# Kernel optimization log

Hardware: AMD Instinct MI355X
Metric: run time of the kernel (lower is better)

## Reference

```python
import jax, jax.numpy as jnp
import numpy as np

B, NI, NP, A, R, D, SH = 1024, 256, 131072, 32, 8, 28, 9
WHITE_BKGD = True

C0 = 0.28209479177387814
C1 = 0.4886025119029199
C2 = (1.0925484305920792, -1.0925484305920792, 0.31539156525252005,
      -1.0925484305920792, 0.5462742152960396)

def sh_basis(dirs):
    # real SH basis, degree 2 (9 components), on normalized directions
    d = dirs / jnp.linalg.norm(dirs, axis=-1, keepdims=True)
    x, y, z = d[..., 0], d[..., 1], d[..., 2]
    return jnp.stack([
        jnp.full_like(x, C0), -C1 * y, C1 * z, -C1 * x,
        C2[0] * x * y, C2[1] * y * z, C2[2] * (2.0 * z * z - x * x - y * y),
        C2[3] * x * z, C2[4] * (x * x - y * y)], axis=-1)

def setup_inputs():
    key = jax.random.key(0)
    k0, k1, k2, k3, k4 = jax.random.split(key, 5)
    rays_d = jax.random.normal(k0, (B, 3), dtype=jnp.float32)
    queries = 0.1 * jax.random.normal(k1, (NP, A), dtype=jnp.float32)
    intrs_pts = jax.random.uniform(k2, (NP, 3), dtype=jnp.float32)
    intersections = 2.0 + 4.0 * jnp.sort(
        jax.random.uniform(k3, (B, NI + 1), dtype=jnp.float32), axis=1)
    atoms = 0.05 * jax.random.normal(k4, (A, R ** 3, D), dtype=jnp.float32)
    atoms = atoms.at[..., -1].add(0.1)  # init_sigma on density channel
    idx = np.sort(np.random.default_rng(0).choice(B * NI, NP, replace=False)).astype(np.int32)
    return {"rays_d": rays_d, "queries": queries, "intrs_pts": intrs_pts,
            "intersections": intersections, "atoms": atoms,
            "scatter_idx": jnp.asarray(idx)}

def reference(rays_d, queries, intrs_pts, intersections, atoms, scatter_idx):
    # ---- l2_interp: dictionary-atom trilinear interpolation ----
    pts = intrs_pts * 2.0 - 1.0                                  # [-1,1]^3 (in-place mul/sub in torch)
    coord = jnp.clip((pts + 1.0) * 0.5 * (R - 1), 0.0, R - 1)    # align_corners grid coords
    i0 = jnp.clip(jnp.floor(coord).astype(jnp.int32), 0, R - 2)
    f = coord - i0.astype(coord.dtype)                            # [NP,3] fractional offsets
    data = jnp.zeros((NP, D), dtype=queries.dtype)
    for dx in (0, 1):
        for dy in (0, 1):
            for dz in (0, 1):
                idx = ((i0[:, 0] + dx) * R + (i0[:, 1] + dy)) * R + (i0[:, 2] + dz)
                w = ((f[:, 0] if dx else 1.0 - f[:, 0]) *
                     (f[:, 1] if dy else 1.0 - f[:, 1]) *
                     (f[:, 2] if dz else 1.0 - f[:, 2]))
                g = atoms[:, idx, :]                              # [A, NP, D]
                data = data + jnp.einsum('pa,apd->pd', queries * w[:, None], g)
    # ---- density: masked_scatter + relu ----
    sigma_m = data[:, -1]
    sigma = jnp.zeros((B * NI,), sigma_m.dtype).at[scatter_idx].set(sigma_m).reshape(B, NI)
    sigma = jax.nn.relu(sigma)
    # ---- sigma2alpha: alpha compositing weights ----
    dists = jnp.diff(intersections, axis=1) * jnp.linalg.norm(rays_d, axis=-1, keepdims=True)
    alpha = 1.0 - jnp.exp(-sigma * dists)                         # [B, NI]
    trans = jnp.cumprod(1.0 - alpha + 1e-10, axis=1)
    trans = jnp.concatenate([jnp.ones((B, 1), alpha.dtype), trans[:, :-1]], axis=1)
    abs_light = alpha * trans
    # ---- SH shading on masked points ----
    sh_m = sh_basis(rays_d)[scatter_idx // NI]                    # [NP, SH] (gather via ray index)
    rgb_m = jnp.sum(sh_m[:, None, :] * data[:, :-1].reshape(NP, 3, SH), axis=-1)
    rgb = jnp.zeros((B * NI, 3), rgb_m.dtype).at[scatter_idx].set(rgb_m).reshape(B, NI, 3)
    # ---- shrgb2rgb ----
    rgb = jax.nn.sigmoid(rgb)
    acc = jnp.sum(abs_light, axis=1)
    rgb_out = jnp.sum(abs_light[..., None] * rgb, axis=1)
    if WHITE_BKGD:
        rgb_out = rgb_out + (1.0 - acc)[:, None]
    # ---- depth_map ----
    mid = 0.5 * (intersections[:, :-1] + intersections[:, 1:])
    depth = jnp.sum(abs_light * mid, axis=1)
    return rgb_out, alpha, depth
```

## Files before the change

kernel.cpp:

```cpp
#include <hip/hip_runtime.h>

#define NPTS  131072
#define NB    1024
#define NI    256
#define NA    32
#define RR    8
#define ND    28
#define NCELL 343
#define CAP   768
#define NCHUNKS 3
#define CHUNK 256

typedef _Float16 half8v __attribute__((ext_vector_type(8)));
typedef float    f32x4  __attribute__((ext_vector_type(4)));

__device__ __forceinline__ void cell_coords(const float* __restrict__ ip, int p,
                                            int& ix, int& iy, int& iz) {
  float cx = fminf(fmaxf(ip[p * 3 + 0] * 7.f, 0.f), 7.f);
  float cy = fminf(fmaxf(ip[p * 3 + 1] * 7.f, 0.f), 7.f);
  float cz = fminf(fmaxf(ip[p * 3 + 2] * 7.f, 0.f), 7.f);
  ix = (int)floorf(cx); ix = ix > 6 ? 6 : ix;
  iy = (int)floorf(cy); iy = iy > 6 ? 6 : iy;
  iz = (int)floorf(cz); iz = iz > 6 ? 6 : iz;
}

__global__ __launch_bounds__(256) void init_transpose(const float* __restrict__ atoms,
                                                      _Float16* __restrict__ atomsH,
                                                      f32x4* __restrict__ zbuf,
                                                      int* __restrict__ cnt) {
  int idx = blockIdx.x * 256 + threadIdx.x;
  int vox = idx >> 10;
  int d = (idx >> 5) & 31;
  int a = idx & 31;
  float v = 0.f;
  if (d < ND) v = atoms[(a * 512 + vox) * ND + d];
  atomsH[idx] = (_Float16)v;
  if (idx < NB * NI) {
    f32x4 z = {0.f, 0.f, 0.f, 0.f};
    zbuf[idx] = z;
  }
  if (idx < NCELL) cnt[idx] = 0;
}

__global__ __launch_bounds__(256) void scatter_kernel(const float* __restrict__ ip,
                                                      int* __restrict__ cnt,
                                                      int* __restrict__ perm) {
  __shared__ int sc[NCELL];
  __shared__ int sbase[NCELL];
  for (int c = threadIdx.x; c < NCELL; c += 256) sc[c] = 0;
  __syncthreads();
  int mycell[4], myrank[4], myp[4];
#pragma unroll
  for (int u = 0; u < 4; u++) {
    int p = blockIdx.x * 1024 + u * 256 + threadIdx.x;
    int ix, iy, iz;
    cell_coords(ip, p, ix, iy, iz);
    int cell = (ix * 7 + iy) * 7 + iz;
    mycell[u] = cell;
    myp[u] = p;
    myrank[u] = atomicAdd(&sc[cell], 1);
  }
  __syncthreads();
  for (int c = threadIdx.x; c < NCELL; c += 256) {
    int n = sc[c];
    sbase[c] = n ? atomicAdd(&cnt[c], n) : 0;
  }
  __syncthreads();
#pragma unroll
  for (int u = 0; u < 4; u++)
    perm[mycell[u] * CAP + sbase[mycell[u]] + myrank[u]] = myp[u];
}

__global__ __launch_bounds__(256) void gemm_points(
    const int* __restrict__ cnt, const int* __restrict__ perm,
    const float* __restrict__ queries, const float* __restrict__ intrs_pts,
    const float* __restrict__ rays_d, const int* __restrict__ scatter_idx,
    const _Float16* __restrict__ atomsH,
    float* __restrict__ sigma_d, float* __restrict__ rgb_d) {
  int cell = blockIdx.x / NCHUNKS;
  int chunk = blockIdx.x - cell * NCHUNKS;
  int n = cnt[cell];
  int s0 = chunk * CHUNK;
  if (s0 >= n) return;
  int e0 = min(n, s0 + CHUNK);
  const int* pcell = perm + cell * CAP;

  int cx = cell / 49, cy = (cell / 7) % 7, cz = cell % 7;

  __shared__ _Float16 Bs[8 * 32 * 32];
  __shared__ float Ds[4][16][33];

  int t = threadIdx.x;
#pragma unroll
  for (int u = 0; u < 4; u++) {
    int chk = t + u * 256;
    int g = chk << 3;
    int c = g >> 10;
    int rem = g & 1023;
    int d = rem >> 5;
    int kg = (rem >> 3) & 3;
    int vox = ((cx + (c >> 2)) * RR + cy + ((c >> 1) & 1)) * RR + cz + (c & 1);
    const _Float16* src = atomsH + vox * 1024 + d * 32 + (kg << 3);
    int swz = kg ^ ((d >> 1) & 3);
    _Float16* dst = (_Float16*)Bs + c * 1024 + d * 32 + (swz << 3);
    *(half8v*)dst = *(const half8v*)src;
  }
  __syncthreads();

  int lane = t & 63, w = t >> 6;
  int n0 = lane & 15, kg = lane >> 4;

  half8v Bf[8][2];
#pragma unroll
  for (int s = 0; s < 8; s++)
#pragma unroll
    for (int dt = 0; dt < 2; dt++) {
      int nn = n0 + 16 * dt;
      int swz = kg ^ ((nn >> 1) & 3);
      Bf[s][dt] = *(const half8v*)((const _Float16*)Bs + (s * 32 + nn) * 32 + (swz << 3));
    }

  for (int tile = 0; tile < 4; tile++) {
    int pbase = s0 + w * 64 + tile * 16;
    if (pbase >= e0) break;
    int pidx = pbase + n0;
    bool valid = pidx < e0;
    int p = valid ? pcell[pidx] : 0;

    float cxv = fminf(fmaxf(intrs_pts[p * 3 + 0] * 7.f, 0.f), 7.f);
    float cyv = fminf(fmaxf(intrs_pts[p * 3 + 1] * 7.f, 0.f), 7.f);
    float czv = fminf(fmaxf(intrs_pts[p * 3 + 2] * 7.f, 0.f), 7.f);
    float fx = cxv - (float)cx;
    float fy = cyv - (float)cy;
    float fz = czv - (float)cz;
    float vm = valid ? 1.f : 0.f;

    float wgt[8];
#pragma unroll
    for (int s = 0; s < 8; s++)
      wgt[s] = vm * ((s & 4) ? fx : 1.f - fx) * ((s & 2) ? fy : 1.f - fy) *
               ((s & 1) ? fz : 1.f - fz);

    f32x4 q0 = *(const f32x4*)(queries + p * NA + kg * 8);
    f32x4 q1 = *(const f32x4*)(queries + p * NA + kg * 8 + 4);
    half8v qh;
    qh[0] = (_Float16)q0[0]; qh[1] = (_Float16)q0[1];
    qh[2] = (_Float16)q0[2]; qh[3] = (_Float16)q0[3];
    qh[4] = (_Float16)q1[0]; qh[5] = (_Float16)q1[1];
    qh[6] = (_Float16)q1[2]; qh[7] = (_Float16)q1[3];

    f32x4 acc0 = {0.f, 0.f, 0.f, 0.f};
    f32x4 acc1 = {0.f, 0.f, 0.f, 0.f};
#pragma unroll
    for (int s = 0; s < 8; s++) {
      _Float16 wh = (_Float16)wgt[s];
      half8v ws8 = {wh, wh, wh, wh, wh, wh, wh, wh};
      half8v af = qh * ws8;
      acc0 = __builtin_amdgcn_mfma_f32_16x16x32_f16(af, Bf[s][0], acc0, 0, 0, 0);
      acc1 = __builtin_amdgcn_mfma_f32_16x16x32_f16(af, Bf[s][1], acc1, 0, 0, 0);
    }

#pragma unroll
    for (int r = 0; r < 4; r++) {
      Ds[w][kg * 4 + r][n0]      = acc0[r];
      Ds[w][kg * 4 + r][n0 + 16] = acc1[r];
    }

    int m16 = n0, o = kg;
    int pe = pbase + m16;
    if (pe < e0) {
      int p2 = pcell[pe];
      int sidx = scatter_idx[p2];
      if (o == 3) {
        sigma_d[sidx] = Ds[w][m16][27];
      } else {
        int b = sidx >> 8;
        float rxv = rays_d[b * 3 + 0], ryv = rays_d[b * 3 + 1], rzv = rays_d[b * 3 + 2];
        float inv = rsqrtf(rxv * rxv + ryv * ryv + rzv * rzv);
        float X = rxv * inv, Y = ryv * inv, Z = rzv * inv;
        float shb[9];
        shb[0] = 0.28209479177387814f;
        shb[1] = -0.4886025119029199f * Y;
        shb[2] = 0.4886025119029199f * Z;
        shb[3] = -0.4886025119029199f * X;
        shb[4] = 1.0925484305920792f * X * Y;
        shb[5] = -1.0925484305920792f * Y * Z;
        shb[6] = 0.31539156525252005f * (2.f * Z * Z - X * X - Y * Y);
        shb[7] = -1.0925484305920792f * X * Z;
        shb[8] = 0.5462742152960396f * (X * X - Y * Y);
        float sum = 0.f;
#pragma unroll
        for (int sh = 0; sh < 9; sh++) sum += shb[sh] * Ds[w][m16][o * 9 + sh];
        rgb_d[(size_t)sidx * 3 + o] = sum;
      }
    }
  }
}

__global__ __launch_bounds__(256) void ray_kernel(
    const float* __restrict__ intersections, const float* __restrict__ rays_d,
    const float* __restrict__ sigma_d, const float* __restrict__ rgb_d,
    float* __restrict__ out) {
  int b = blockIdx.x;
  int i = threadIdx.x;
  int wid = i >> 6;
  int lane = i & 63;

  float t0 = intersections[b * (NI + 1) + i];
  float t1 = intersections[b * (NI + 1) + i + 1];
  float rxv = rays_d[b * 3 + 0], ryv = rays_d[b * 3 + 1], rzv = rays_d[b * 3 + 2];
  float nrm = sqrtf(rxv * rxv + ryv * ryv + rzv * rzv);
  float dist = (t1 - t0) * nrm;
  float mid = 0.5f * (t0 + t1);

  float sg = fmaxf(sigma_d[b * NI + i], 0.f);
  float alpha = 1.f - expf(-sg * dist);
  out[3072 + b * NI + i] = alpha;

  float x = 1.f - alpha + 1e-10f;

  float v = x;
#pragma unroll
  for (int off = 1; off < 64; off <<= 1) {
    float tv = __shfl_up(v, off, 64);
    if (lane >= off) v *= tv;
  }
  __shared__ float wtot[4];
  if (lane == 63) wtot[wid] = v;
  __syncthreads();
  float pre = 1.f;
  for (int w2 = 0; w2 < wid; w2++) pre *= wtot[w2];
  float vprev = __shfl_up(v, 1, 64);
  float trans = (lane == 0) ? pre : pre * vprev;
  float al = alpha * trans;

  float r0 = rgb_d[(size_t)(b * NI + i) * 3 + 0];
  float r1 = rgb_d[(size_t)(b * NI + i) * 3 + 1];
  float r2 = rgb_d[(size_t)(b * NI + i) * 3 + 2];
  float g0 = 1.f / (1.f + expf(-r0));
  float g1 = 1.f / (1.f + expf(-r1));
  float g2 = 1.f / (1.f + expf(-r2));

  float v0 = al, v1 = al * mid, v2 = al * g0, v3 = al * g1, v4 = al * g2;
#pragma unroll
  for (int off = 1; off < 64; off <<= 1) {
    v0 += __shfl_xor(v0, off, 64);
    v1 += __shfl_xor(v1, off, 64);
    v2 += __shfl_xor(v2, off, 64);
    v3 += __shfl_xor(v3, off, 64);
    v4 += __shfl_xor(v4, off, 64);
  }
  __shared__ float wred[4][5];
  if (lane == 0) {
    wred[wid][0] = v0; wred[wid][1] = v1; wred[wid][2] = v2;
    wred[wid][3] = v3; wred[wid][4] = v4;
  }
  __syncthreads();
  if (i == 0) {
    float a0 = 0.f, a1 = 0.f, a2 = 0.f, a3 = 0.f, a4 = 0.f;
#pragma unroll
    for (int w = 0; w < 4; w++) {
      a0 += wred[w][0]; a1 += wred[w][1]; a2 += wred[w][2];
      a3 += wred[w][3]; a4 += wred[w][4];
    }
    float white = 1.f - a0;
    out[b * 3 + 0] = a2 + white;
    out[b * 3 + 1] = a3 + white;
    out[b * 3 + 2] = a4 + white;
    out[3072 + NB * NI + b] = a1;
  }
}

extern "C" void kernel_launch(void* const* d_in, const int* in_sizes, int n_in,
                              void* d_out, int out_size, void* d_ws, size_t ws_size,
                              hipStream_t stream) {
  const float* rays_d        = (const float*)d_in[0];
  const float* queries       = (const float*)d_in[1];
  const float* intrs_pts     = (const float*)d_in[2];
  const float* intersections = (const float*)d_in[3];
  const float* atoms         = (const float*)d_in[4];
  const int*   scatter_idx   = (const int*)d_in[5];
  float* out = (float*)d_out;

  float*    sigma_d = (float*)d_ws;
  float*    rgb_d   = sigma_d + NB * NI;
  _Float16* atomsH  = (_Float16*)(rgb_d + (size_t)NB * NI * 3);
  int*      perm    = (int*)(atomsH + 512 * 1024);
  int*      cnt     = perm + NCELL * CAP;

  init_transpose<<<2048, 256, 0, stream>>>(atoms, atomsH, (f32x4*)d_ws, cnt);
  scatter_kernel<<<128, 256, 0, stream>>>(intrs_pts, cnt, perm);
  gemm_points<<<NCELL * NCHUNKS, 256, 0, stream>>>(cnt, perm, queries, intrs_pts,
                                                   rays_d, scatter_idx, atomsH,
                                                   sigma_d, rgb_d);
  ray_kernel<<<NB, 256, 0, stream>>>(intersections, rays_d, sigma_d, rgb_d, out);
}
```

Baseline: 36.14 us.

## Drop LDS staging of atom tiles and shrink per-block point chunks

The point GEMM kernel no longer stages the 8-corner atom tile into shared memory. Each wave now loads its B fragments directly from global (L2-resident) fp16 atoms and handles one 16-point tile, not four. The chunk size drops from 256 to 64 points per block, so there are four times as many, smaller blocks. This removes the LDS fill, the barrier and the per-block staging latency and raises parallelism, at the cost of repeated global/L2 reads of the same atom data across waves and blocks.

```diff
diff --git a/kernel.cpp b/kernel.cpp
--- a/kernel.cpp
+++ b/kernel.cpp
@@ -8,8 +8,8 @@
 #define ND    28
 #define NCELL 343
 #define CAP   768
-#define NCHUNKS 3
-#define CHUNK 256
+#define NCHUNKS 12
+#define CHUNK 64
 
 typedef _Float16 half8v __attribute__((ext_vector_type(8)));
 typedef float    f32x4  __attribute__((ext_vector_type(4)));
@@ -35,10 +35,7 @@
   float v = 0.f;
   if (d < ND) v = atoms[(a * 512 + vox) * ND + d];
   atomsH[idx] = (_Float16)v;
-  if (idx < NB * NI) {
-    f32x4 z = {0.f, 0.f, 0.f, 0.f};
-    zbuf[idx] = z;
-  }
+  if (idx < NB * NI) { f32x4 z = {0.f, 0.f, 0.f, 0.f}; zbuf[idx] = z; }
   if (idx < NCELL) cnt[idx] = 0;
 }
 
@@ -84,115 +81,90 @@
   if (s0 >= n) return;
   int e0 = min(n, s0 + CHUNK);
   const int* pcell = perm + cell * CAP;
-
   int cx = cell / 49, cy = (cell / 7) % 7, cz = cell % 7;
 
-  __shared__ _Float16 Bs[8 * 32 * 32];
   __shared__ float Ds[4][16][33];
 
   int t = threadIdx.x;
-#pragma unroll
-  for (int u = 0; u < 4; u++) {
-    int chk = t + u * 256;
-    int g = chk << 3;
-    int c = g >> 10;
-    int rem = g & 1023;
-    int d = rem >> 5;
-    int kg = (rem >> 3) & 3;
-    int vox = ((cx + (c >> 2)) * RR + cy + ((c >> 1) & 1)) * RR + cz + (c & 1);
-    const _Float16* src = atomsH + vox * 1024 + d * 32 + (kg << 3);
-    int swz = kg ^ ((d >> 1) & 3);
-    _Float16* dst = (_Float16*)Bs + c * 1024 + d * 32 + (swz << 3);
-    *(half8v*)dst = *(const half8v*)src;
-  }
-  __syncthreads();
-
   int lane = t & 63, w = t >> 6;
   int n0 = lane & 15, kg = lane >> 4;
 
-  half8v Bf[8][2];
+  int pbase = s0 + w * 16;
+  if (pbase >= e0) return;
+
+  int pidx = pbase + n0;
+  bool valid = pidx < e0;
+  int p = valid ? pcell[pidx] : 0;
+
+  float cxv = fminf(fmaxf(intrs_pts[p * 3 + 0] * 7.f, 0.f), 7.f);
+  float cyv = fminf(fmaxf(intrs_pts[p * 3 + 1] * 7.f, 0.f), 7.f);
+  float czv = fminf(fmaxf(intrs_pts[p * 3 + 2] * 7.f, 0.f), 7.f);
+  float fx = cxv - (float)cx;
+  float fy = cyv - (float)cy;
+  float fz = czv - (float)cz;
+  float vm = valid ? 1.f : 0.f;
+
+  float wgt[8];
 #pragma unroll
   for (int s = 0; s < 8; s++)
-#pragma unroll
-    for (int dt = 0; dt < 2; dt++) {
-      int nn = n0 + 16 * dt;
-      int swz = kg ^ ((nn >> 1) & 3);
-      Bf[s][dt] = *(const half8v*)((const _Float16*)Bs + (s * 32 + nn) * 32 + (swz << 3));
-    }
-
-  for (int tile = 0; tile < 4; tile++) {
-    int pbase = s0 + w * 64 + tile * 16;
-    if (pbase >= e0) break;
-    int pidx = pbase + n0;
-    bool valid = pidx < e0;
-    int p = valid ? pcell[pidx] : 0;
-
-    float cxv = fminf(fmaxf(intrs_pts[p * 3 + 0] * 7.f, 0.f), 7.f);
-    float cyv = fminf(fmaxf(intrs_pts[p * 3 + 1] * 7.f, 0.f), 7.f);
-    float czv = fminf(fmaxf(intrs_pts[p * 3 + 2] * 7.f, 0.f), 7.f);
-    float fx = cxv - (float)cx;
-    float fy = cyv - (float)cy;
-    float fz = czv - (float)cz;
-    float vm = valid ? 1.f : 0.f;
-
-    float wgt[8];
-#pragma unroll
-    for (int s = 0; s < 8; s++)
-      wgt[s] = vm * ((s & 4) ? fx : 1.f - fx) * ((s & 2) ? fy : 1.f - fy) *
-               ((s & 1) ? fz : 1.f - fz);
-
-    f32x4 q0 = *(const f32x4*)(queries + p * NA + kg * 8);
-    f32x4 q1 = *(const f32x4*)(queries + p * NA + kg * 8 + 4);
-    half8v qh;
-    qh[0] = (_Float16)q0[0]; qh[1] = (_Float16)q0[1];
-    qh[2] = (_Float16)q0[2]; qh[3] = (_Float16)q0[3];
-    qh[4] = (_Float16)q1[0]; qh[5] = (_Float16)q1[1];
-    qh[6] = (_Float16)q1[2]; qh[7] = (_Float16)q1[3];
-
-    f32x4 acc0 = {0.f, 0.f, 0.f, 0.f};
-    f32x4 acc1 = {0.f, 0.f, 0.f, 0.f};
-#pragma unroll
-    for (int s = 0; s < 8; s++) {
-      _Float16 wh = (_Float16)wgt[s];
-      half8v ws8 = {wh, wh, wh, wh, wh, wh, wh, wh};
-      half8v af = qh * ws8;
-      acc0 = __builtin_amdgcn_mfma_f32_16x16x32_f16(af, Bf[s][0], acc0, 0, 0, 0);
-      acc1 = __builtin_amdgcn_mfma_f32_16x16x32_f16(af, Bf[s][1], acc1, 0, 0, 0);
-    }
-
-#pragma unroll
-    for (int r = 0; r < 4; r++) {
-      Ds[w][kg * 4 + r][n0]      = acc0[r];
-      Ds[w][kg * 4 + r][n0 + 16] = acc1[r];
-    }
-
-    int m16 = n0, o = kg;
-    int pe = pbase + m16;
-    if (pe < e0) {
-      int p2 = pcell[pe];
-      int sidx = scatter_idx[p2];
-      if (o == 3) {
-        sigma_d[sidx] = Ds[w][m16][27];
-      } else {
-        int b = sidx >> 8;
-        float rxv = rays_d[b * 3 + 0], ryv = rays_d[b * 3 + 1], rzv = rays_d[b * 3 + 2];
-        float inv = rsqrtf(rxv * rxv + ryv * ryv + rzv * rzv);
-        float X = rxv * inv, Y = ryv * inv, Z = rzv * inv;
-        float shb[9];
-        shb[0] = 0.28209479177387814f;
-        shb[1] = -0.4886025119029199f * Y;
-        shb[2] = 0.4886025119029199f * Z;
-        shb[3] = -0.4886025119029199f * X;
-        shb[4] = 1.0925484305920792f * X * Y;
-        shb[5] = -1.0925484305920792f * Y * Z;
-        shb[6] = 0.31539156525252005f * (2.f * Z * Z - X * X - Y * Y);
-        shb[7] = -1.0925484305920792f * X * Z;
-        shb[8] = 0.5462742152960396f * (X * X - Y * Y);
-        float sum = 0.f;
-#pragma unroll
-        for (int sh = 0; sh < 9; sh++) sum += shb[sh] * Ds[w][m16][o * 9 + sh];
-        rgb_d[(size_t)sidx * 3 + o] = sum;
-      }
+    wgt[s] = vm * ((s & 4) ? fx : 1.f - fx) * ((s & 2) ? fy : 1.f - fy) *
+             ((s & 1) ? fz : 1.f - fz);
+
+  f32x4 q0 = *(const f32x4*)(queries + p * NA + kg * 8);
+  f32x4 q1 = *(const f32x4*)(queries + p * NA + kg * 8 + 4);
+  half8v qh;
+  qh[0] = (_Float16)q0[0]; qh[1] = (_Float16)q0[1];
+  qh[2] = (_Float16)q0[2]; qh[3] = (_Float16)q0[3];
+  qh[4] = (_Float16)q1[0]; qh[5] = (_Float16)q1[1];
+  qh[6] = (_Float16)q1[2]; qh[7] = (_Float16)q1[3];
+
+  f32x4 acc0 = {0.f, 0.f, 0.f, 0.f};
+  f32x4 acc1 = {0.f, 0.f, 0.f, 0.f};
+#pragma unroll
+  for (int s = 0; s < 8; s++) {
+    int vox = ((cx + (s >> 2)) * RR + cy + ((s >> 1) & 1)) * RR + cz + (s & 1);
+    const _Float16* bp = atomsH + vox * 1024 + kg * 8;
+    half8v b0 = *(const half8v*)(bp + n0 * 32);
+    half8v b1 = *(const half8v*)(bp + (n0 + 16) * 32);
+    _Float16 wh = (_Float16)wgt[s];
+    half8v ws8 = {wh, wh, wh, wh, wh, wh, wh, wh};
+    half8v af = qh * ws8;
+    acc0 = __builtin_amdgcn_mfma_f32_16x16x32_f16(af, b0, acc0, 0, 0, 0);
+    acc1 = __builtin_amdgcn_mfma_f32_16x16x32_f16(af, b1, acc1, 0, 0, 0);
+  }
+
+#pragma unroll
+  for (int r = 0; r < 4; r++) {
+    Ds[w][kg * 4 + r][n0]      = acc0[r];
+    Ds[w][kg * 4 + r][n0 + 16] = acc1[r];
+  }
+
+  int m16 = n0, o = kg;
+  int pe = pbase + m16;
+  if (pe < e0) {
+    int p2 = pcell[pe];
+    int sidx = scatter_idx[p2];
+    if (o == 3) {
+      sigma_d[sidx] = Ds[w][m16][27];
+    } else {
+      int b = sidx >> 8;
+      float rxv = rays_d[b * 3 + 0], ryv = rays_d[b * 3 + 1], rzv = rays_d[b * 3 + 2];
+      float inv = rsqrtf(rxv * rxv + ryv * ryv + rzv * rzv);
+      float X = rxv * inv, Y = ryv * inv, Z = rzv * inv;
+      float shb[9];
+      shb[0] = 0.28209479177387814f;
+      shb[1] = -0.4886025119029199f * Y;
+      shb[2] = 0.4886025119029199f * Z;
+      shb[3] = -0.4886025119029199f * X;
+      shb[4] = 1.0925484305920792f * X * Y;
+      shb[5] = -1.0925484305920792f * Y * Z;
+      shb[6] = 0.31539156525252005f * (2.f * Z * Z - X * X - Y * Y);
+      shb[7] = -1.0925484305920792f * X * Z;
+      shb[8] = 0.5462742152960396f * (X * X - Y * Y);
+      float sum = 0.f;
+#pragma unroll
+      for (int sh = 0; sh < 9; sh++) sum += shb[sh] * Ds[w][m16][o * 9 + sh];
+      rgb_d[(size_t)sidx * 3 + o] = sum;
     }
   }
 }
@@ -218,7 +190,6 @@
   out[3072 + b * NI + i] = alpha;
 
   float x = 1.f - alpha + 1e-10f;
-
   float v = x;
 #pragma unroll
   for (int off = 1; off < 64; off <<= 1) {
@@ -259,9 +230,9 @@
   if (i == 0) {
     float a0 = 0.f, a1 = 0.f, a2 = 0.f, a3 = 0.f, a4 = 0.f;
 #pragma unroll
-    for (int w = 0; w < 4; w++) {
-      a0 += wred[w][0]; a1 += wred[w][1]; a2 += wred[w][2];
-      a3 += wred[w][3]; a4 += wred[w][4];
+    for (int w2 = 0; w2 < 4; w2++) {
+      a0 += wred[w2][0]; a1 += wred[w2][1]; a2 += wred[w2][2];
+      a3 += wred[w2][3]; a4 += wred[w2][4];
     }
     float white = 1.f - a0;
     out[b * 3 + 0] = a2 + white;
```

Measured after the change: 41.43 us. 14.6% more time.
